# Optimization experiments

Hardware: AMD Instinct MI355X
Metric: run time of the kernel (lower is better)

The kernel has to match this reference:

```python
import jax, jax.numpy as jnp
import numpy as np

N = 100000   # nodes
E = 1600000  # edges
D_IN, D_H, D_OUT = 128, 128, 64
BN_EPS = 1e-5


def setup_inputs() -> dict:
    key = jax.random.key(0)
    ks = jax.random.split(key, 12)

    def lin_w(k, fan_in, shape):
        s = 1.0 / np.sqrt(fan_in)
        return jax.random.uniform(k, shape, jnp.float32, -s, s)

    return {
        "x": jax.random.normal(ks[0], (N, D_IN), jnp.float32),
        "edge_index": jax.random.randint(ks[1], (2, E), 0, N, dtype=jnp.int64),
        "edge_weight": jax.random.uniform(ks[2], (E,), jnp.float32),
        "W1": lin_w(ks[3], D_IN, (D_IN, D_H)),
        "b1": jnp.zeros((D_H,), jnp.float32),
        "W2": lin_w(ks[4], D_H, (D_H, D_H)),
        "b2": jnp.zeros((D_H,), jnp.float32),
        "W3": lin_w(ks[5], D_H, (D_H, D_OUT)),
        "b3": jnp.zeros((D_OUT,), jnp.float32),
        "gamma1": jnp.ones((D_H,), jnp.float32),
        "beta1": jnp.zeros((D_H,), jnp.float32),
        "gamma2": jnp.ones((D_H,), jnp.float32),
        "beta2": jnp.zeros((D_H,), jnp.float32),
    }


def _gcn_conv(x, src, dst, w, W, b):
    # PyG GCNConv: x' = D^{-1/2} (A + I) D^{-1/2} (x W) + b, self-loop weight 1
    n = x.shape[0]
    h = x @ W                                   # [N, d_out]
    loop = jnp.arange(n, dtype=src.dtype)
    s = jnp.concatenate([src, loop])            # [E+N]
    d = jnp.concatenate([dst, loop])
    ww = jnp.concatenate([w, jnp.ones((n,), w.dtype)])
    deg = jax.ops.segment_sum(ww, d, num_segments=n)          # in-degree at targets
    dinv = jnp.where(deg > 0, jax.lax.rsqrt(deg), 0.0)
    norm = dinv[s] * ww * dinv[d]               # [E+N]
    msg = h[s] * norm[:, None]                  # gather + scale
    out = jax.ops.segment_sum(msg, d, num_segments=n)
    return out + b


def _batch_norm(x, gamma, beta):
    mean = jnp.mean(x, axis=0)
    var = jnp.mean(jnp.square(x - mean), axis=0)  # biased, as BatchNorm uses
    return (x - mean) * jax.lax.rsqrt(var + BN_EPS) * gamma + beta


def reference(x, edge_index, edge_weight, W1, b1, W2, b2, W3, b3,
              gamma1, beta1, gamma2, beta2):
    src, dst = edge_index[0], edge_index[1]
    h = _gcn_conv(x, src, dst, edge_weight, W1, b1)
    h = jax.nn.relu(_batch_norm(h, gamma1, beta1))
    h = _gcn_conv(h, src, dst, edge_weight, W2, b2)
    h = jax.nn.relu(_batch_norm(h, gamma2, beta2))
    return _gcn_conv(h, src, dst, edge_weight, W3, b3)
```

## Files before the change

kernel.cpp:

```cpp
#include <hip/hip_runtime.h>
#include <hip/hip_fp16.h>
#include <cstdint>
#include <cstddef>

#define BN_EPS 1e-5f
#define FPSCALE 268435456.0f

typedef _Float16 half8 __attribute__((ext_vector_type(8)));
typedef float floatx4 __attribute__((ext_vector_type(4)));

__device__ __forceinline__ float loadS(const __half* p) { return __half2float(*p); }
__device__ __forceinline__ float2 load2(const __half* p) {
    return __half22float2(*(const __half2*)p);
}
__device__ __forceinline__ void storeS(float* p, float v) { *p = v; }
__device__ __forceinline__ void storeS(__half* p, float v) { *p = __float2half(v); }
__device__ __forceinline__ void store2(float* p, float a, float b) {
    *(float2*)p = make_float2(a, b);
}
__device__ __forceinline__ void store2(__half* p, float a, float b) {
    *(__half2*)p = __floats2half2_rn(a, b);
}
__device__ __forceinline__ float wn_of(unsigned v) {
    __half_raw hr; hr.x = (unsigned short)(v & 0x7fffu);
    return __half2float((__half)hr);
}

static __device__ __forceinline__ int load_edge(const void* ei, int mode64, long long pos) {
    if (mode64) return (int)((const long long*)ei)[pos];
    return ((const int*)ei)[pos];
}

__global__ __launch_bounds__(256) void init_kernel(const unsigned* __restrict__ eiw, int nwords,
                                                   int* __restrict__ mode,
                                                   unsigned long long* __restrict__ packed, int N,
                                                   const float* __restrict__ W1,
                                                   const float* __restrict__ W2,
                                                   const float* __restrict__ W3,
                                                   _Float16* __restrict__ WT1,
                                                   _Float16* __restrict__ WT2,
                                                   _Float16* __restrict__ WT3, int nb) {
    __shared__ unsigned red[256];
    const int bid = (int)blockIdx.x;
    const int tid = (int)threadIdx.x;
    if (bid < nb) {
        int i = bid * 256 + tid;
        if (i < N) packed[i] = 0ULL;
        return;
    }
    if (bid == nb) {
        unsigned m = 0;
        for (int i = 1 + 2 * tid; i < nwords; i += 512) m |= eiw[i];
        red[tid] = m;
        __syncthreads();
        for (int s = 128; s > 0; s >>= 1) {
            if (tid < s) red[tid] |= red[tid + s];
            __syncthreads();
        }
        if (tid == 0) mode[0] = (red[0] == 0) ? 1 : 0;
        return;
    }
    const int t_ = bid - nb - 1;
    if (t_ < 64) {
        int t = t_ * 256 + tid;
        int n = t / 128, k = t % 128;
        WT1[t] = (_Float16)W1[k * 128 + n];
    } else if (t_ < 128) {
        int t = (t_ - 64) * 256 + tid;
        int n = t / 128, k = t % 128;
        WT2[t] = (_Float16)W2[k * 128 + n];
    } else {
        int t = (t_ - 128) * 256 + tid;
        int n = t / 128, k = t % 128;
        WT3[t] = (_Float16)W3[k * 64 + n];
    }
}

template <int M, bool BN, typename TI>
__device__ __forceinline__ void gemm_body(int gbid, const TI* __restrict__ X,
                                          const _Float16* __restrict__ WTg,
                                          const float* __restrict__ sc,
                                          const float* __restrict__ sh,
                                          __half* __restrict__ Hout, int N,
                                          _Float16* WT ) {
    constexpr int CT = M / 16;
    constexpr int LDK = 136;

    for (int t = threadIdx.x; t < M * 16; t += 256) {
        int n = t / 16, seg = t % 16;
        *(half8*)&WT[n * LDK + seg * 8] = *(const half8*)&WTg[n * 128 + seg * 8];
    }
    __syncthreads();

    const int wave = (int)threadIdx.x >> 6;
    const int lane = (int)threadIdx.x & 63;
    const int qd = lane >> 4;
    const int ln = lane & 15;
    const int tile0 = gbid * 64 + wave * 16;
    int ar = tile0 + ln;
    if (ar >= N) ar = N - 1;

    half8 aF[4];
    const TI* xr = X + (size_t)ar * 128 + qd * 8;
#pragma unroll
    for (int kb = 0; kb < 4; ++kb) {
        float vv[8];
        if constexpr (sizeof(TI) == 4) {
            float4 v0 = *(const float4*)(xr + kb * 32);
            float4 v1 = *(const float4*)(xr + kb * 32 + 4);
            vv[0] = v0.x; vv[1] = v0.y; vv[2] = v0.z; vv[3] = v0.w;
            vv[4] = v1.x; vv[5] = v1.y; vv[6] = v1.z; vv[7] = v1.w;
        } else {
            half8 raw = *(const half8*)(xr + kb * 32);
#pragma unroll
            for (int j = 0; j < 8; ++j) vv[j] = (float)raw[j];
        }
        if (BN) {
            const int kbase = kb * 32 + qd * 8;
#pragma unroll
            for (int j = 0; j < 8; ++j)
                vv[j] = fmaxf(fmaf(vv[j], sc[kbase + j], sh[kbase + j]), 0.0f);
        }
        half8 a;
#pragma unroll
        for (int j = 0; j < 8; ++j) a[j] = (_Float16)vv[j];
        aF[kb] = a;
    }

#pragma unroll
    for (int ct = 0; ct < CT; ++ct) {
        floatx4 acc = {0.0f, 0.0f, 0.0f, 0.0f};
#pragma unroll
        for (int kb = 0; kb < 4; ++kb) {
            half8 b = *(const half8*)&WT[(ct * 16 + ln) * LDK + kb * 32 + qd * 8];
            acc = __builtin_amdgcn_mfma_f32_16x16x32_f16(aF[kb], b, acc, 0, 0, 0);
        }
#pragma unroll
        for (int r = 0; r < 4; ++r) {
            int orow = tile0 + qd * 4 + r;
            if (orow < N) Hout[(size_t)orow * M + ct * 16 + ln] = __float2half(acc[r]);
        }
    }
}

__global__ __launch_bounds__(256) void hist_gemm1_kernel(const void* __restrict__ ei,
                                                         const float* __restrict__ ew,
                                                         unsigned long long* __restrict__ packed,
                                                         unsigned* __restrict__ rank,
                                                         const int* __restrict__ mode, int E, int GB,
                                                         const float* __restrict__ X,
                                                         const _Float16* __restrict__ WT1g,
                                                         __half* __restrict__ Hout, int N) {
    __shared__ _Float16 WT[128 * 136];
    if ((int)blockIdx.x < GB) {
        gemm_body<128, false, float>(blockIdx.x, X, WT1g, nullptr, nullptr, Hout, N, WT);
        return;
    }
    int e = ((int)blockIdx.x - GB) * 256 + (int)threadIdx.x;
    if (e >= E) return;
    int md = *mode;
    int d = load_edge(ei, md, (long long)E + e);
    unsigned long long contrib = (1ULL << 40) | (unsigned long long)(ew[e] * FPSCALE);
    unsigned long long old = atomicAdd(&packed[d], contrib);
    rank[e] = (unsigned)(old >> 40);
}

__global__ __launch_bounds__(256) void unpack_scanA_kernel(const unsigned long long* __restrict__ packed,
                                                           float* __restrict__ dinv,
                                                           int* __restrict__ cnt,
                                                           int* __restrict__ bsum, int N) {
    __shared__ int red[256];
    const int tid = (int)threadIdx.x;
    const int base = (int)blockIdx.x * 2048 + tid * 8;
    int s = 0;
#pragma unroll
    for (int j = 0; j < 8; ++j) {
        int idx = base + j;
        if (idx < N) {
            unsigned long long p = packed[idx];
            int c = (int)(p >> 40);
            cnt[idx] = c;
            dinv[idx] = rsqrtf(1.0f + (float)(p & 0xFFFFFFFFFFULL) * (1.0f / FPSCALE));
            s += c;
        }
    }
    red[tid] = s;
    __syncthreads();
    for (int st = 128; st > 0; st >>= 1) {
        if (tid < st) red[tid] += red[tid + st];
        __syncthreads();
    }
    if (tid == 0) bsum[blockIdx.x] = red[0];
}

__global__ __launch_bounds__(256) void scanC_kernel(const int* __restrict__ cnt,
                                                    const int* __restrict__ bsum,
                                                    int* __restrict__ row_start, int N) {
    __shared__ int lds[256];
    const int tid = (int)threadIdx.x;
    int gbase = 0;
    for (int j = 0; j < (int)blockIdx.x; ++j) gbase += bsum[j];
    const int base = (int)blockIdx.x * 2048 + tid * 8;
    int vals[8];
    int s = 0;
#pragma unroll
    for (int j = 0; j < 8; ++j) {
        int idx = base + j;
        int v = (idx < N) ? cnt[idx] : 0;
        vals[j] = s;
        s += v;
    }
    lds[tid] = s;
    __syncthreads();
    for (int off = 1; off < 256; off <<= 1) {
        int t = 0;
        if (tid >= off) t = lds[tid - off];
        __syncthreads();
        lds[tid] += t;
        __syncthreads();
    }
    int excl = lds[tid] - s;
    int b = gbase + excl;
#pragma unroll
    for (int j = 0; j < 8; ++j) {
        int idx = base + j;
        if (idx < N) row_start[idx] = b + vals[j];
    }
}

__global__ __launch_bounds__(256) void scatter_zero_kernel(const void* __restrict__ ei,
                                                           const float* __restrict__ ew,
                                                           const float* __restrict__ dinv,
                                                           const int* __restrict__ row_start,
                                                           const unsigned* __restrict__ rank,
                                                           unsigned* __restrict__ edata,
                                                           const int* __restrict__ mode, int E, int EBK,
                                                           float* __restrict__ gsum,
                                                           float* __restrict__ gsq) {
    if ((int)blockIdx.x == EBK) {
        if (threadIdx.x < 128) { gsum[threadIdx.x] = 0.0f; gsq[threadIdx.x] = 0.0f; }
        return;
    }
    int e = (int)blockIdx.x * 256 + (int)threadIdx.x;
    if (e >= E) return;
    int md = *mode;
    int s = load_edge(ei, md, e);
    int d = load_edge(ei, md, (long long)E + e);
    float wn = dinv[s] * ew[e] * dinv[d];
    unsigned hb = (unsigned)__half_as_ushort(__float2half(wn)) & 0x7fffu;
    edata[row_start[d] + (int)rank[e]] = ((unsigned)s << 15) | hb;
}

template <int D, bool BIAS, typename TY>
__global__ __launch_bounds__(256) void agg_kernel(const __half* __restrict__ H,
                                                  const unsigned* __restrict__ edata,
                                                  const int* __restrict__ row_start,
                                                  const int* __restrict__ cnt,
                                                  const float* __restrict__ dinv,
                                                  const float* __restrict__ bias,
                                                  TY* __restrict__ Y, int N) {
    constexpr int VPT = D / 64;
    const int lane = (int)threadIdx.x & 63;
    const int i = (int)blockIdx.x * 4 + ((int)threadIdx.x >> 6);
    if (i >= N) return;
    const int c0 = lane * VPT;
    const float di = dinv[i];
    const float dii = di * di;

    float acc0, acc1 = 0.0f;
    if constexpr (VPT == 2) {
        float2 h = load2(H + (size_t)i * D + c0);
        acc0 = dii * h.x;
        acc1 = dii * h.y;
    } else {
        acc0 = dii * loadS(H + (size_t)i * D + c0);
    }

    const int base = row_start[i];
    const int n = cnt[i];
    for (int off = 0; off < n; off += 64) {
        const int rem = n - off;
        unsigned ev = 0;
        if (lane < rem) ev = edata[base + off + lane];
        const int mm = min(64, rem);
        for (int j = 0; j < mm; j += 8) {
            const unsigned e0 = __shfl(ev, j),     e1 = __shfl(ev, j + 1);
            const unsigned e2 = __shfl(ev, j + 2), e3 = __shfl(ev, j + 3);
            const unsigned e4 = __shfl(ev, j + 4), e5 = __shfl(ev, j + 5);
            const unsigned e6 = __shfl(ev, j + 6), e7 = __shfl(ev, j + 7);
            if constexpr (VPT == 2) {
                float2 h0 = load2(H + (size_t)(e0 >> 15) * D + c0);
                float2 h1 = load2(H + (size_t)(e1 >> 15) * D + c0);
                float2 h2 = load2(H + (size_t)(e2 >> 15) * D + c0);
                float2 h3 = load2(H + (size_t)(e3 >> 15) * D + c0);
                float2 h4 = load2(H + (size_t)(e4 >> 15) * D + c0);
                float2 h5 = load2(H + (size_t)(e5 >> 15) * D + c0);
                float2 h6 = load2(H + (size_t)(e6 >> 15) * D + c0);
                float2 h7 = load2(H + (size_t)(e7 >> 15) * D + c0);
                acc0 = fmaf(wn_of(e0), h0.x, acc0); acc1 = fmaf(wn_of(e0), h0.y, acc1);
                acc0 = fmaf(wn_of(e1), h1.x, acc0); acc1 = fmaf(wn_of(e1), h1.y, acc1);
                acc0 = fmaf(wn_of(e2), h2.x, acc0); acc1 = fmaf(wn_of(e2), h2.y, acc1);
                acc0 = fmaf(wn_of(e3), h3.x, acc0); acc1 = fmaf(wn_of(e3), h3.y, acc1);
                acc0 = fmaf(wn_of(e4), h4.x, acc0); acc1 = fmaf(wn_of(e4), h4.y, acc1);
                acc0 = fmaf(wn_of(e5), h5.x, acc0); acc1 = fmaf(wn_of(e5), h5.y, acc1);
                acc0 = fmaf(wn_of(e6), h6.x, acc0); acc1 = fmaf(wn_of(e6), h6.y, acc1);
                acc0 = fmaf(wn_of(e7), h7.x, acc0); acc1 = fmaf(wn_of(e7), h7.y, acc1);
            } else {
                float h0 = loadS(H + (size_t)(e0 >> 15) * D + c0);
                float h1 = loadS(H + (size_t)(e1 >> 15) * D + c0);
                float h2 = loadS(H + (size_t)(e2 >> 15) * D + c0);
                float h3 = loadS(H + (size_t)(e3 >> 15) * D + c0);
                float h4 = loadS(H + (size_t)(e4 >> 15) * D + c0);
                float h5 = loadS(H + (size_t)(e5 >> 15) * D + c0);
                float h6 = loadS(H + (size_t)(e6 >> 15) * D + c0);
                float h7 = loadS(H + (size_t)(e7 >> 15) * D + c0);
                acc0 = fmaf(wn_of(e0), h0, acc0);
                acc0 = fmaf(wn_of(e1), h1, acc0);
                acc0 = fmaf(wn_of(e2), h2, acc0);
                acc0 = fmaf(wn_of(e3), h3, acc0);
                acc0 = fmaf(wn_of(e4), h4, acc0);
                acc0 = fmaf(wn_of(e5), h5, acc0);
                acc0 = fmaf(wn_of(e6), h6, acc0);
                acc0 = fmaf(wn_of(e7), h7, acc0);
            }
        }
    }

    if constexpr (VPT == 2) {
        if (BIAS) { acc0 += bias[c0]; acc1 += bias[c0 + 1]; }
        store2(Y + (size_t)i * D + c0, acc0, acc1);
    } else {
        if (BIAS) acc0 += bias[c0];
        storeS(Y + (size_t)i * D + c0, acc0);
    }
}

template <int M, bool BN, typename TI, bool ZERO>
__global__ __launch_bounds__(256) void gemm_mfma_kernel(const TI* __restrict__ X,
                                                        const _Float16* __restrict__ WTg,
                                                        const float* __restrict__ sc,
                                                        const float* __restrict__ sh,
                                                        __half* __restrict__ Hout, int N,
                                                        float* __restrict__ gsum,
                                                        float* __restrict__ gsq, int GB) {
    __shared__ _Float16 WT[M * 136];
    if (ZERO && (int)blockIdx.x == GB) {
        if (threadIdx.x < 128) { gsum[threadIdx.x] = 0.0f; gsq[threadIdx.x] = 0.0f; }
        return;
    }
    gemm_body<M, BN, TI>(blockIdx.x, X, WTg, sc, sh, Hout, N, WT);
}

__global__ void stats_kernel(const __half* __restrict__ Y, float* __restrict__ gsum,
                             float* __restrict__ gsq, int N) {
    __shared__ float ls[256], lq[256];
    const int tid = threadIdx.x;
    const int c = tid & 127;
    const int half_ = tid >> 7;
    float s = 0.0f, q = 0.0f;
    for (int row = blockIdx.x * 2 + half_; row < N; row += 512) {
        float v = __half2float(Y[(size_t)row * 128 + c]);
        s += v;
        q = fmaf(v, v, q);
    }
    ls[tid] = s; lq[tid] = q;
    __syncthreads();
    if (tid < 128) {
        atomicAdd(&gsum[c], ls[tid] + ls[tid + 128]);
        atomicAdd(&gsq[c],  lq[tid] + lq[tid + 128]);
    }
}

__global__ void finalize_stats_kernel(const float* __restrict__ gsum, const float* __restrict__ gsq,
                                      const float* __restrict__ gamma, const float* __restrict__ beta,
                                      float* __restrict__ sc, float* __restrict__ sh, int N) {
    int t = threadIdx.x;
    if (t < 128) {
        float inv_n = 1.0f / (float)N;
        float mean = gsum[t] * inv_n;
        float var = gsq[t] * inv_n - mean * mean;
        float scale = gamma[t] * rsqrtf(var + BN_EPS);
        sc[t] = scale;
        sh[t] = beta[t] - mean * scale;
    }
}

extern "C" void kernel_launch(void* const* d_in, const int* in_sizes, int n_in,
                              void* d_out, int out_size, void* d_ws, size_t ws_size,
                              hipStream_t stream) {
    const float* x   = (const float*)d_in[0];
    const void*  ei  = d_in[1];
    const float* ew  = (const float*)d_in[2];
    const float* W1  = (const float*)d_in[3];
    const float* W2  = (const float*)d_in[5];
    const float* W3  = (const float*)d_in[7];
    const float* b3  = (const float*)d_in[8];
    const float* g1  = (const float*)d_in[9];
    const float* be1 = (const float*)d_in[10];
    const float* g2  = (const float*)d_in[11];
    const float* be2 = (const float*)d_in[12];
    float* out = (float*)d_out;

    const int N = in_sizes[0] / 128;
    const int E = in_sizes[2];
    const int G = (N + 2047) / 2048;

    char* w = (char*)d_ws;
    size_t off = 0;
    auto alloc = [&](size_t bytes) -> void* {
        void* p = w + off;
        off += (bytes + 255) & ~(size_t)255;
        return p;
    };
    unsigned long long* packed = (unsigned long long*)alloc((size_t)N * 8);
    float* dinv      = (float*)alloc((size_t)N * 4);
    int*   cnt       = (int*)  alloc((size_t)N * 4);
    int*   row_start = (int*)  alloc((size_t)N * 4);
    unsigned* rank   = (unsigned*)alloc((size_t)E * 4);
    unsigned* edata  = (unsigned*)alloc((size_t)E * 4);
    int*   bsum      = (int*)  alloc((size_t)G * 4);
    int*   mode      = (int*)  alloc(256);
    float* gsum      = (float*)alloc(128 * 4);
    float* gsq       = (float*)alloc(128 * 4);
    float* scb       = (float*)alloc(128 * 4);
    float* shb       = (float*)alloc(128 * 4);
    _Float16* WT1    = (_Float16*)alloc(128 * 128 * 2);
    _Float16* WT2    = (_Float16*)alloc(128 * 128 * 2);
    _Float16* WT3    = (_Float16*)alloc(128 * 64 * 2);
    __half* H        = (__half*)alloc((size_t)N * 128 * 2);
    __half* Yh       = (__half*)alloc((size_t)N * 128 * 2);
    (void)ws_size; (void)n_in; (void)out_size;

    const int nb  = (N + 255) / 256;
    const int ebk = (E + 255) / 256;
    const int gb  = (N + 63) / 64;
    const int ab  = (N + 3) / 4;

    init_kernel<<<nb + 1 + 160, 256, 0, stream>>>((const unsigned*)ei, 4096, mode, packed, N,
                                                  W1, W2, W3, WT1, WT2, WT3, nb);
    hist_gemm1_kernel<<<gb + ebk, 256, 0, stream>>>(ei, ew, packed, rank, mode, E, gb,
                                                    x, WT1, H, N);
    unpack_scanA_kernel<<<G, 256, 0, stream>>>(packed, dinv, cnt, bsum, N);
    scanC_kernel<<<G, 256, 0, stream>>>(cnt, bsum, row_start, N);
    scatter_zero_kernel<<<ebk + 1, 256, 0, stream>>>(ei, ew, dinv, row_start, rank, edata,
                                                     mode, E, ebk, gsum, gsq);

    agg_kernel<128, false, __half><<<ab, 256, 0, stream>>>(H, edata, row_start, cnt, dinv, nullptr, Yh, N);
    stats_kernel<<<256, 256, 0, stream>>>(Yh, gsum, gsq, N);
    finalize_stats_kernel<<<1, 128, 0, stream>>>(gsum, gsq, g1, be1, scb, shb, N);

    gemm_mfma_kernel<128, true, __half, true><<<gb + 1, 256, 0, stream>>>(Yh, WT2, scb, shb, H, N, gsum, gsq, gb);
    agg_kernel<128, false, __half><<<ab, 256, 0, stream>>>(H, edata, row_start, cnt, dinv, nullptr, Yh, N);
    stats_kernel<<<256, 256, 0, stream>>>(Yh, gsum, gsq, N);
    finalize_stats_kernel<<<1, 128, 0, stream>>>(gsum, gsq, g2, be2, scb, shb, N);

    gemm_mfma_kernel<64, true, __half, false><<<gb, 256, 0, stream>>>(Yh, WT3, scb, shb, H, N, nullptr, nullptr, gb);
    agg_kernel<64, true, float><<<ab, 256, 0, stream>>>(H, edata, row_start, cnt, dinv, b3, out, N);
}
```

Baseline: 550.6 us.

## Pad degree counters, vectorize histogram atomics, drop LDS from fused GEMM1

Each node's packed degree/count atomic now gets its own 64-byte slot, which is meant to cut contention and false sharing between neighbouring atomics. Each histogram thread now handles four edges with vector loads of indices, weights and rank stores. The first GEMM reads the FP16 weights straight from global memory instead of staging them in a 34KB LDS tile. That lets the kernel declare a higher occupancy hint and puts histogram blocks first in the grid. In exchange the packed array is eight times larger, so the zero-init and unpack reads become strided and touch more memory.

```diff
diff --git a/kernel.cpp b/kernel.cpp
--- a/kernel.cpp
+++ b/kernel.cpp
@@ -5,6 +5,7 @@
 
 #define BN_EPS 1e-5f
 #define FPSCALE 268435456.0f
+#define PPS 8
 
 typedef _Float16 half8 __attribute__((ext_vector_type(8)));
 typedef float floatx4 __attribute__((ext_vector_type(4)));
@@ -45,7 +46,7 @@
     const int tid = (int)threadIdx.x;
     if (bid < nb) {
         int i = bid * 256 + tid;
-        if (i < N) packed[i] = 0ULL;
+        if (i < N) packed[(size_t)i * PPS] = 0ULL;
         return;
     }
     if (bid == nb) {
@@ -143,26 +144,98 @@
     }
 }
 
-__global__ __launch_bounds__(256) void hist_gemm1_kernel(const void* __restrict__ ei,
-                                                         const float* __restrict__ ew,
-                                                         unsigned long long* __restrict__ packed,
-                                                         unsigned* __restrict__ rank,
-                                                         const int* __restrict__ mode, int E, int GB,
-                                                         const float* __restrict__ X,
-                                                         const _Float16* __restrict__ WT1g,
-                                                         __half* __restrict__ Hout, int N) {
-    __shared__ _Float16 WT[128 * 136];
-    if ((int)blockIdx.x < GB) {
-        gemm_body<128, false, float>(blockIdx.x, X, WT1g, nullptr, nullptr, Hout, N, WT);
+__device__ __forceinline__ void gemm1_nolds(int gbid, const float* __restrict__ X,
+                                            const _Float16* __restrict__ WTg,
+                                            __half* __restrict__ Hout, int N) {
+    const int wave = (int)threadIdx.x >> 6;
+    const int lane = (int)threadIdx.x & 63;
+    const int qd = lane >> 4;
+    const int ln = lane & 15;
+    const int tile0 = gbid * 64 + wave * 16;
+    int ar = tile0 + ln;
+    if (ar >= N) ar = N - 1;
+
+    half8 aF[4];
+    const float* xr = X + (size_t)ar * 128 + qd * 8;
+#pragma unroll
+    for (int kb = 0; kb < 4; ++kb) {
+        float4 v0 = *(const float4*)(xr + kb * 32);
+        float4 v1 = *(const float4*)(xr + kb * 32 + 4);
+        half8 a;
+        a[0] = (_Float16)v0.x; a[1] = (_Float16)v0.y;
+        a[2] = (_Float16)v0.z; a[3] = (_Float16)v0.w;
+        a[4] = (_Float16)v1.x; a[5] = (_Float16)v1.y;
+        a[6] = (_Float16)v1.z; a[7] = (_Float16)v1.w;
+        aF[kb] = a;
+    }
+
+#pragma unroll 1
+    for (int ct = 0; ct < 8; ++ct) {
+        floatx4 acc = {0.0f, 0.0f, 0.0f, 0.0f};
+#pragma unroll
+        for (int kb = 0; kb < 4; ++kb) {
+            half8 b = *(const half8*)&WTg[(size_t)(ct * 16 + ln) * 128 + kb * 32 + qd * 8];
+            acc = __builtin_amdgcn_mfma_f32_16x16x32_f16(aF[kb], b, acc, 0, 0, 0);
+        }
+#pragma unroll
+        for (int r = 0; r < 4; ++r) {
+            int orow = tile0 + qd * 4 + r;
+            if (orow < N) Hout[(size_t)orow * 128 + ct * 16 + ln] = __float2half(acc[r]);
+        }
+    }
+}
+
+__global__ __launch_bounds__(256, 8) void hist_gemm1_kernel(const void* __restrict__ ei,
+                                                            const float* __restrict__ ew,
+                                                            unsigned long long* __restrict__ packed,
+                                                            unsigned* __restrict__ rank,
+                                                            const int* __restrict__ mode, int E, int HB,
+                                                            const float* __restrict__ X,
+                                                            const _Float16* __restrict__ WT1g,
+                                                            __half* __restrict__ Hout, int N) {
+    if ((int)blockIdx.x >= HB) {
+        gemm1_nolds((int)blockIdx.x - HB, X, WT1g, Hout, N);
         return;
     }
-    int e = ((int)blockIdx.x - GB) * 256 + (int)threadIdx.x;
-    if (e >= E) return;
-    int md = *mode;
-    int d = load_edge(ei, md, (long long)E + e);
-    unsigned long long contrib = (1ULL << 40) | (unsigned long long)(ew[e] * FPSCALE);
-    unsigned long long old = atomicAdd(&packed[d], contrib);
-    rank[e] = (unsigned)(old >> 40);
+    const int md = *mode;
+    const int e = (int)blockIdx.x * 1024 + (int)threadIdx.x * 4;
+    if (e + 3 < E) {
+        long long d0, d1, d2, d3;
+        if (md) {
+            const long long* p = (const long long*)ei + (long long)E + e;
+            longlong2 a = *(const longlong2*)p;
+            longlong2 b = *(const longlong2*)(p + 2);
+            d0 = a.x; d1 = a.y; d2 = b.x; d3 = b.y;
+        } else {
+            const int* p = (const int*)ei + (long long)E + e;
+            int4 a = *(const int4*)p;
+            d0 = a.x; d1 = a.y; d2 = a.z; d3 = a.w;
+        }
+        float4 w4 = *(const float4*)(ew + e);
+        unsigned long long o0 = atomicAdd(&packed[(size_t)d0 * PPS],
+                                          (1ULL << 40) | (unsigned long long)(w4.x * FPSCALE));
+        unsigned long long o1 = atomicAdd(&packed[(size_t)d1 * PPS],
+                                          (1ULL << 40) | (unsigned long long)(w4.y * FPSCALE));
+        unsigned long long o2 = atomicAdd(&packed[(size_t)d2 * PPS],
+                                          (1ULL << 40) | (unsigned long long)(w4.z * FPSCALE));
+        unsigned long long o3 = atomicAdd(&packed[(size_t)d3 * PPS],
+                                          (1ULL << 40) | (unsigned long long)(w4.w * FPSCALE));
+        uint4 r4;
+        r4.x = (unsigned)(o0 >> 40); r4.y = (unsigned)(o1 >> 40);
+        r4.z = (unsigned)(o2 >> 40); r4.w = (unsigned)(o3 >> 40);
+        *(uint4*)(rank + e) = r4;
+    } else {
+#pragma unroll 1
+        for (int k = 0; k < 4; ++k) {
+            int ee = e + k;
+            if (ee >= E) break;
+            int d = load_edge(ei, md, (long long)E + ee);
+            unsigned long long contrib =
+                (1ULL << 40) | (unsigned long long)(ew[ee] * FPSCALE);
+            unsigned long long old = atomicAdd(&packed[(size_t)d * PPS], contrib);
+            rank[ee] = (unsigned)(old >> 40);
+        }
+    }
 }
 
 __global__ __launch_bounds__(256) void unpack_scanA_kernel(const unsigned long long* __restrict__ packed,
@@ -177,7 +250,7 @@
     for (int j = 0; j < 8; ++j) {
         int idx = base + j;
         if (idx < N) {
-            unsigned long long p = packed[idx];
+            unsigned long long p = packed[(size_t)idx * PPS];
             int c = (int)(p >> 40);
             cnt[idx] = c;
             dinv[idx] = rsqrtf(1.0f + (float)(p & 0xFFFFFFFFFFULL) * (1.0f / FPSCALE));
@@ -412,7 +485,7 @@
         off += (bytes + 255) & ~(size_t)255;
         return p;
     };
-    unsigned long long* packed = (unsigned long long*)alloc((size_t)N * 8);
+    unsigned long long* packed = (unsigned long long*)alloc((size_t)N * 8 * PPS);
     float* dinv      = (float*)alloc((size_t)N * 4);
     int*   cnt       = (int*)  alloc((size_t)N * 4);
     int*   row_start = (int*)  alloc((size_t)N * 4);
@@ -433,12 +506,13 @@
 
     const int nb  = (N + 255) / 256;
     const int ebk = (E + 255) / 256;
+    const int ehb = (E + 1023) / 1024;
     const int gb  = (N + 63) / 64;
     const int ab  = (N + 3) / 4;
 
     init_kernel<<<nb + 1 + 160, 256, 0, stream>>>((const unsigned*)ei, 4096, mode, packed, N,
                                                   W1, W2, W3, WT1, WT2, WT3, nb);
-    hist_gemm1_kernel<<<gb + ebk, 256, 0, stream>>>(ei, ew, packed, rank, mode, E, gb,
+    hist_gemm1_kernel<<<ehb + gb, 256, 0, stream>>>(ei, ew, packed, rank, mode, E, ehb,
                                                     x, WT1, H, N);
     unpack_scanA_kernel<<<G, 256, 0, stream>>>(packed, dinv, cnt, bsum, N);
     scanC_kernel<<<G, 256, 0, stream>>>(cnt, bsum, row_start, N);
```

Measured after the change: 581.8 us. 5.7% more time.

## Privatize degree histogram per XCC with workgroup-scope atomics

Applied to the files above, without the earlier changes.

The packed degree/count histogram is replicated into eight copies, one per XCC selected via the hardware XCC_ID register. Atomics now use workgroup scope so they can resolve in the local L2 instead of device-wide memory. Each thread also handles four edges with vector loads. The unpack step merges the copies and records per-copy prefix offsets so the scatter can compute slots, at the cost of extra zeroing, a larger workspace and an extra offset array read.

```diff
diff --git a/kernel.cpp b/kernel.cpp
--- a/kernel.cpp
+++ b/kernel.cpp
@@ -5,6 +5,7 @@
 
 #define BN_EPS 1e-5f
 #define FPSCALE 268435456.0f
+#define NCOPY 8
 
 typedef _Float16 half8 __attribute__((ext_vector_type(8)));
 typedef float floatx4 __attribute__((ext_vector_type(4)));
@@ -29,6 +30,12 @@
 static __device__ __forceinline__ int load_edge(const void* ei, int mode64, long long pos) {
     if (mode64) return (int)((const long long*)ei)[pos];
     return ((const int*)ei)[pos];
+}
+
+__device__ __forceinline__ unsigned xcc_id() {
+    unsigned v;
+    asm volatile("s_getreg_b32 %0, hwreg(HW_REG_XCC_ID)" : "=s"(v));
+    return v & 7u;
 }
 
 __global__ __launch_bounds__(256) void init_kernel(const unsigned* __restrict__ eiw, int nwords,
@@ -44,8 +51,15 @@
     const int bid = (int)blockIdx.x;
     const int tid = (int)threadIdx.x;
     if (bid < nb) {
-        int i = bid * 256 + tid;
-        if (i < N) packed[i] = 0ULL;
+        const size_t tot = (size_t)NCOPY * (size_t)N;
+        size_t i = (size_t)bid * 1024 + (size_t)tid * 4;
+        if (i + 3 < tot) {
+            *(ulonglong2*)&packed[i]     = make_ulonglong2(0ULL, 0ULL);
+            *(ulonglong2*)&packed[i + 2] = make_ulonglong2(0ULL, 0ULL);
+        } else {
+            for (int k = 0; k < 4; ++k)
+                if (i + k < tot) packed[i + k] = 0ULL;
+        }
         return;
     }
     if (bid == nb) {
@@ -156,18 +170,60 @@
         gemm_body<128, false, float>(blockIdx.x, X, WT1g, nullptr, nullptr, Hout, N, WT);
         return;
     }
-    int e = ((int)blockIdx.x - GB) * 256 + (int)threadIdx.x;
-    if (e >= E) return;
-    int md = *mode;
-    int d = load_edge(ei, md, (long long)E + e);
-    unsigned long long contrib = (1ULL << 40) | (unsigned long long)(ew[e] * FPSCALE);
-    unsigned long long old = atomicAdd(&packed[d], contrib);
-    rank[e] = (unsigned)(old >> 40);
+    const int md = *mode;
+    const unsigned xcc = xcc_id();
+    unsigned long long* __restrict__ pb = packed + (size_t)xcc * (size_t)N;
+    const int e = ((int)blockIdx.x - GB) * 1024 + (int)threadIdx.x * 4;
+    if (e + 3 < E) {
+        long long d0, d1, d2, d3;
+        if (md) {
+            const long long* p = (const long long*)ei + (long long)E + e;
+            longlong2 a = *(const longlong2*)p;
+            longlong2 b = *(const longlong2*)(p + 2);
+            d0 = a.x; d1 = a.y; d2 = b.x; d3 = b.y;
+        } else {
+            const int* p = (const int*)ei + (long long)E + e;
+            int4 a = *(const int4*)p;
+            d0 = a.x; d1 = a.y; d2 = a.z; d3 = a.w;
+        }
+        float4 w4 = *(const float4*)(ew + e);
+        unsigned long long o0 = __hip_atomic_fetch_add(
+            &pb[d0], (1ULL << 40) | (unsigned long long)(w4.x * FPSCALE),
+            __ATOMIC_RELAXED, __HIP_MEMORY_SCOPE_WORKGROUP);
+        unsigned long long o1 = __hip_atomic_fetch_add(
+            &pb[d1], (1ULL << 40) | (unsigned long long)(w4.y * FPSCALE),
+            __ATOMIC_RELAXED, __HIP_MEMORY_SCOPE_WORKGROUP);
+        unsigned long long o2 = __hip_atomic_fetch_add(
+            &pb[d2], (1ULL << 40) | (unsigned long long)(w4.z * FPSCALE),
+            __ATOMIC_RELAXED, __HIP_MEMORY_SCOPE_WORKGROUP);
+        unsigned long long o3 = __hip_atomic_fetch_add(
+            &pb[d3], (1ULL << 40) | (unsigned long long)(w4.w * FPSCALE),
+            __ATOMIC_RELAXED, __HIP_MEMORY_SCOPE_WORKGROUP);
+        uint4 r4;
+        r4.x = (xcc << 24) | (unsigned)((o0 >> 40) & 0xFFFFFFu);
+        r4.y = (xcc << 24) | (unsigned)((o1 >> 40) & 0xFFFFFFu);
+        r4.z = (xcc << 24) | (unsigned)((o2 >> 40) & 0xFFFFFFu);
+        r4.w = (xcc << 24) | (unsigned)((o3 >> 40) & 0xFFFFFFu);
+        *(uint4*)(rank + e) = r4;
+    } else {
+#pragma unroll 1
+        for (int k = 0; k < 4; ++k) {
+            int ee = e + k;
+            if (ee >= E) break;
+            int d = load_edge(ei, md, (long long)E + ee);
+            unsigned long long contrib =
+                (1ULL << 40) | (unsigned long long)(ew[ee] * FPSCALE);
+            unsigned long long old = __hip_atomic_fetch_add(
+                &pb[d], contrib, __ATOMIC_RELAXED, __HIP_MEMORY_SCOPE_WORKGROUP);
+            rank[ee] = (xcc << 24) | (unsigned)((old >> 40) & 0xFFFFFFu);
+        }
+    }
 }
 
 __global__ __launch_bounds__(256) void unpack_scanA_kernel(const unsigned long long* __restrict__ packed,
                                                            float* __restrict__ dinv,
                                                            int* __restrict__ cnt,
+                                                           unsigned* __restrict__ coff,
                                                            int* __restrict__ bsum, int N) {
     __shared__ int red[256];
     const int tid = (int)threadIdx.x;
@@ -177,11 +233,18 @@
     for (int j = 0; j < 8; ++j) {
         int idx = base + j;
         if (idx < N) {
-            unsigned long long p = packed[idx];
-            int c = (int)(p >> 40);
-            cnt[idx] = c;
-            dinv[idx] = rsqrtf(1.0f + (float)(p & 0xFFFFFFFFFFULL) * (1.0f / FPSCALE));
-            s += c;
+            unsigned long long wsum = 0ULL;
+            unsigned pref = 0;
+#pragma unroll
+            for (int c = 0; c < NCOPY; ++c) {
+                unsigned long long p = packed[(size_t)c * N + idx];
+                coff[(size_t)idx * NCOPY + c] = pref;
+                pref += (unsigned)(p >> 40);
+                wsum += (p & 0xFFFFFFFFFFULL);
+            }
+            cnt[idx] = (int)pref;
+            dinv[idx] = rsqrtf(1.0f + (float)wsum * (1.0f / FPSCALE));
+            s += (int)pref;
         }
     }
     red[tid] = s;
@@ -233,6 +296,7 @@
                                                            const float* __restrict__ dinv,
                                                            const int* __restrict__ row_start,
                                                            const unsigned* __restrict__ rank,
+                                                           const unsigned* __restrict__ coff,
                                                            unsigned* __restrict__ edata,
                                                            const int* __restrict__ mode, int E, int EBK,
                                                            float* __restrict__ gsum,
@@ -248,7 +312,11 @@
     int d = load_edge(ei, md, (long long)E + e);
     float wn = dinv[s] * ew[e] * dinv[d];
     unsigned hb = (unsigned)__half_as_ushort(__float2half(wn)) & 0x7fffu;
-    edata[row_start[d] + (int)rank[e]] = ((unsigned)s << 15) | hb;
+    unsigned r = rank[e];
+    unsigned c = r >> 24;
+    int slot = row_start[d] + (int)coff[(size_t)d * NCOPY + c] + (int)(r & 0xFFFFFFu);
+    slot = min(max(slot, 0), E - 1);
+    edata[slot] = ((unsigned)s << 15) | hb;
 }
 
 template <int D, bool BIAS, typename TY>
@@ -412,12 +480,13 @@
         off += (bytes + 255) & ~(size_t)255;
         return p;
     };
-    unsigned long long* packed = (unsigned long long*)alloc((size_t)N * 8);
+    unsigned long long* packed = (unsigned long long*)alloc((size_t)NCOPY * N * 8);
     float* dinv      = (float*)alloc((size_t)N * 4);
     int*   cnt       = (int*)  alloc((size_t)N * 4);
     int*   row_start = (int*)  alloc((size_t)N * 4);
     unsigned* rank   = (unsigned*)alloc((size_t)E * 4);
     unsigned* edata  = (unsigned*)alloc((size_t)E * 4);
+    unsigned* coff   = (unsigned*)alloc((size_t)N * NCOPY * 4);
     int*   bsum      = (int*)  alloc((size_t)G * 4);
     int*   mode      = (int*)  alloc(256);
     float* gsum      = (float*)alloc(128 * 4);
@@ -431,18 +500,19 @@
     __half* Yh       = (__half*)alloc((size_t)N * 128 * 2);
     (void)ws_size; (void)n_in; (void)out_size;
 
-    const int nb  = (N + 255) / 256;
+    const int nbz = (int)(((size_t)NCOPY * N + 1023) / 1024);
     const int ebk = (E + 255) / 256;
+    const int ehb = (E + 1023) / 1024;
     const int gb  = (N + 63) / 64;
     const int ab  = (N + 3) / 4;
 
-    init_kernel<<<nb + 1 + 160, 256, 0, stream>>>((const unsigned*)ei, 4096, mode, packed, N,
-                                                  W1, W2, W3, WT1, WT2, WT3, nb);
-    hist_gemm1_kernel<<<gb + ebk, 256, 0, stream>>>(ei, ew, packed, rank, mode, E, gb,
+    init_kernel<<<nbz + 1 + 160, 256, 0, stream>>>((const unsigned*)ei, 4096, mode, packed, N,
+                                                   W1, W2, W3, WT1, WT2, WT3, nbz);
+    hist_gemm1_kernel<<<gb + ehb, 256, 0, stream>>>(ei, ew, packed, rank, mode, E, gb,
                                                     x, WT1, H, N);
-    unpack_scanA_kernel<<<G, 256, 0, stream>>>(packed, dinv, cnt, bsum, N);
+    unpack_scanA_kernel<<<G, 256, 0, stream>>>(packed, dinv, cnt, coff, bsum, N);
     scanC_kernel<<<G, 256, 0, stream>>>(cnt, bsum, row_start, N);
-    scatter_zero_kernel<<<ebk + 1, 256, 0, stream>>>(ei, ew, dinv, row_start, rank, edata,
+    scatter_zero_kernel<<<ebk + 1, 256, 0, stream>>>(ei, ew, dinv, row_start, rank, coff, edata,
                                                      mode, E, ebk, gsum, gsq);
 
     agg_kernel<128, false, __half><<<ab, 256, 0, stream>>>(H, edata, row_start, cnt, dinv, nullptr, Yh, N);
```

After: 573.2 us. 1.04x slower.

## Build CSR via two-level bucket sort instead of global per-node atomics

Applied to the files above, without the earlier changes.

Replaces the global 64-bit atomic histogram and rank-based scatter with a coarse bucket sort. Each block first counts edges per 512-node bucket in LDS, the counts are scanned, edges are scattered into bucket order, and a per-bucket kernel builds degree, dinv, row_start and edata using LDS atomics. The edge weight stored in edata no longer includes the source dinv, so the aggregation kernels now gather dinv[src] per edge instead. This removes contended global atomics, at the cost of an extra pass over the edges, a 64-bit sorted buffer and extra dinv gathers in every aggregation.

```diff
diff --git a/kernel.cpp b/kernel.cpp
--- a/kernel.cpp
+++ b/kernel.cpp
@@ -4,7 +4,8 @@
 #include <cstddef>
 
 #define BN_EPS 1e-5f
-#define FPSCALE 268435456.0f
+#define KB 256
+#define BSH 9
 
 typedef _Float16 half8 __attribute__((ext_vector_type(8)));
 typedef float floatx4 __attribute__((ext_vector_type(4)));
@@ -33,22 +34,22 @@
 
 __global__ __launch_bounds__(256) void init_kernel(const unsigned* __restrict__ eiw, int nwords,
                                                    int* __restrict__ mode,
-                                                   unsigned long long* __restrict__ packed, int N,
+                                                   unsigned* __restrict__ pc,
                                                    const float* __restrict__ W1,
                                                    const float* __restrict__ W2,
                                                    const float* __restrict__ W3,
                                                    _Float16* __restrict__ WT1,
                                                    _Float16* __restrict__ WT2,
-                                                   _Float16* __restrict__ WT3, int nb) {
+                                                   _Float16* __restrict__ WT3) {
     __shared__ unsigned red[256];
     const int bid = (int)blockIdx.x;
     const int tid = (int)threadIdx.x;
-    if (bid < nb) {
-        int i = bid * 256 + tid;
-        if (i < N) packed[i] = 0ULL;
+    if (bid < 64) {
+        uint4 z = make_uint4(0, 0, 0, 0);
+        *(uint4*)&pc[bid * 1024 + tid * 4] = z;
         return;
     }
-    if (bid == nb) {
+    if (bid == 64) {
         unsigned m = 0;
         for (int i = 1 + 2 * tid; i < nwords; i += 512) m |= eiw[i];
         red[tid] = m;
@@ -60,7 +61,7 @@
         if (tid == 0) mode[0] = (red[0] == 0) ? 1 : 0;
         return;
     }
-    const int t_ = bid - nb - 1;
+    const int t_ = bid - 65;
     if (t_ < 64) {
         int t = t_ * 256 + tid;
         int n = t / 128, k = t % 128;
@@ -76,6 +77,65 @@
     }
 }
 
+__global__ __launch_bounds__(256) void coarse_hist_kernel(const void* __restrict__ ei,
+                                                          const int* __restrict__ mode,
+                                                          unsigned* __restrict__ pc,
+                                                          int E, int epb) {
+    __shared__ unsigned h[256];
+    const int k = (int)blockIdx.x;
+    const int tid = (int)threadIdx.x;
+    h[tid] = 0;
+    __syncthreads();
+    const int md = *mode;
+    const int e0 = k * epb;
+    const int e1 = min(E, e0 + epb);
+    for (int e = e0 + tid; e < e1; e += 256) {
+        int d = load_edge(ei, md, (long long)E + e);
+        atomicAdd(&h[d >> BSH], 1u);
+    }
+    __syncthreads();
+    pc[k * 256 + tid] = h[tid];
+}
+
+__global__ __launch_bounds__(256) void scan_pc_kernel(unsigned* __restrict__ pc,
+                                                      int* __restrict__ tb) {
+    __shared__ int red[256];
+    const int b = (int)blockIdx.x;
+    const int tid = (int)threadIdx.x;
+    const unsigned v = pc[tid * 256 + b];
+    red[tid] = (int)v;
+    __syncthreads();
+    for (int off = 1; off < 256; off <<= 1) {
+        int t = 0;
+        if (tid >= off) t = red[tid - off];
+        __syncthreads();
+        red[tid] += t;
+        __syncthreads();
+    }
+    pc[tid * 256 + b] = (unsigned)(red[tid] - (int)v);
+    if (tid == 255) tb[b] = red[255];
+}
+
+__global__ __launch_bounds__(256) void scan_buckets_kernel(const int* __restrict__ tb,
+                                                           int* __restrict__ bbase, int nbuck,
+                                                           float* __restrict__ gsum,
+                                                           float* __restrict__ gsq) {
+    __shared__ int red[256];
+    const int tid = (int)threadIdx.x;
+    const int v = (tid < nbuck) ? tb[tid] : 0;
+    red[tid] = v;
+    __syncthreads();
+    for (int off = 1; off < 256; off <<= 1) {
+        int t = 0;
+        if (tid >= off) t = red[tid - off];
+        __syncthreads();
+        red[tid] += t;
+        __syncthreads();
+    }
+    bbase[tid] = red[tid] - v;
+    if (tid < 128) { gsum[tid] = 0.0f; gsq[tid] = 0.0f; }
+}
+
 template <int M, bool BN, typename TI>
 __device__ __forceinline__ void gemm_body(int gbid, const TI* __restrict__ X,
                                           const _Float16* __restrict__ WTg,
@@ -143,112 +203,113 @@
     }
 }
 
-__global__ __launch_bounds__(256) void hist_gemm1_kernel(const void* __restrict__ ei,
+__global__ __launch_bounds__(256) void sort_gemm1_kernel(const void* __restrict__ ei,
                                                          const float* __restrict__ ew,
-                                                         unsigned long long* __restrict__ packed,
-                                                         unsigned* __restrict__ rank,
-                                                         const int* __restrict__ mode, int E, int GB,
+                                                         const unsigned* __restrict__ pc,
+                                                         const int* __restrict__ bbase,
+                                                         unsigned long long* __restrict__ sortedE,
+                                                         const int* __restrict__ mode, int E,
+                                                         int epb, int GB,
                                                          const float* __restrict__ X,
                                                          const _Float16* __restrict__ WT1g,
                                                          __half* __restrict__ Hout, int N) {
     __shared__ _Float16 WT[128 * 136];
+    __shared__ unsigned off_s[256];
     if ((int)blockIdx.x < GB) {
         gemm_body<128, false, float>(blockIdx.x, X, WT1g, nullptr, nullptr, Hout, N, WT);
         return;
     }
-    int e = ((int)blockIdx.x - GB) * 256 + (int)threadIdx.x;
-    if (e >= E) return;
-    int md = *mode;
-    int d = load_edge(ei, md, (long long)E + e);
-    unsigned long long contrib = (1ULL << 40) | (unsigned long long)(ew[e] * FPSCALE);
-    unsigned long long old = atomicAdd(&packed[d], contrib);
-    rank[e] = (unsigned)(old >> 40);
-}
-
-__global__ __launch_bounds__(256) void unpack_scanA_kernel(const unsigned long long* __restrict__ packed,
-                                                           float* __restrict__ dinv,
-                                                           int* __restrict__ cnt,
-                                                           int* __restrict__ bsum, int N) {
+    const int k = (int)blockIdx.x - GB;
+    const int tid = (int)threadIdx.x;
+    off_s[tid] = (unsigned)bbase[tid] + pc[k * 256 + tid];
+    __syncthreads();
+    const int md = *mode;
+    const int e0 = k * epb;
+    const int e1 = min(E, e0 + epb);
+    for (int e = e0 + tid; e < e1; e += 256) {
+        int d = load_edge(ei, md, (long long)E + e);
+        int s = load_edge(ei, md, e);
+        float wv = ew[e];
+        unsigned slot = atomicAdd(&off_s[d >> BSH], 1u);
+        sortedE[slot] = ((unsigned long long)(unsigned)d << 33) |
+                        ((unsigned long long)(unsigned)s << 16) |
+                        (unsigned long long)(unsigned short)__half_as_ushort(__float2half(wv));
+    }
+}
+
+__global__ __launch_bounds__(256) void csr_build_kernel(const unsigned long long* __restrict__ sortedE,
+                                                        const int* __restrict__ bbase,
+                                                        const int* __restrict__ tb,
+                                                        float* __restrict__ dinv,
+                                                        int* __restrict__ cnt,
+                                                        int* __restrict__ row_start,
+                                                        unsigned* __restrict__ edata, int N) {
+    __shared__ unsigned cs[512];
+    __shared__ float ws[512];
+    __shared__ float dv[512];
+    __shared__ unsigned sc[512];
+    __shared__ unsigned cur[512];
     __shared__ int red[256];
+    const int b = (int)blockIdx.x;
     const int tid = (int)threadIdx.x;
-    const int base = (int)blockIdx.x * 2048 + tid * 8;
-    int s = 0;
-#pragma unroll
-    for (int j = 0; j < 8; ++j) {
-        int idx = base + j;
-        if (idx < N) {
-            unsigned long long p = packed[idx];
-            int c = (int)(p >> 40);
-            cnt[idx] = c;
-            dinv[idx] = rsqrtf(1.0f + (float)(p & 0xFFFFFFFFFFULL) * (1.0f / FPSCALE));
-            s += c;
-        }
-    }
-    red[tid] = s;
-    __syncthreads();
-    for (int st = 128; st > 0; st >>= 1) {
-        if (tid < st) red[tid] += red[tid + st];
-        __syncthreads();
-    }
-    if (tid == 0) bsum[blockIdx.x] = red[0];
-}
-
-__global__ __launch_bounds__(256) void scanC_kernel(const int* __restrict__ cnt,
-                                                    const int* __restrict__ bsum,
-                                                    int* __restrict__ row_start, int N) {
-    __shared__ int lds[256];
-    const int tid = (int)threadIdx.x;
-    int gbase = 0;
-    for (int j = 0; j < (int)blockIdx.x; ++j) gbase += bsum[j];
-    const int base = (int)blockIdx.x * 2048 + tid * 8;
-    int vals[8];
-    int s = 0;
-#pragma unroll
-    for (int j = 0; j < 8; ++j) {
-        int idx = base + j;
-        int v = (idx < N) ? cnt[idx] : 0;
-        vals[j] = s;
-        s += v;
-    }
-    lds[tid] = s;
+    const int n0 = b << BSH;
+    const int base = bbase[b];
+    const int len = tb[b];
+
+    cs[tid] = 0; cs[tid + 256] = 0;
+    ws[tid] = 0.0f; ws[tid + 256] = 0.0f;
+    cur[tid] = 0; cur[tid + 256] = 0;
+    __syncthreads();
+
+    for (int i = tid; i < len; i += 256) {
+        unsigned long long p = sortedE[base + i];
+        unsigned fine = (unsigned)(p >> 33) - (unsigned)n0;
+        atomicAdd(&cs[fine], 1u);
+        __half_raw hr; hr.x = (unsigned short)(p & 0xFFFFu);
+        atomicAdd(&ws[fine], __half2float((__half)hr));
+    }
+    __syncthreads();
+
+    const unsigned a0 = cs[2 * tid];
+    const unsigned a1 = cs[2 * tid + 1];
+    const int s2 = (int)(a0 + a1);
+    red[tid] = s2;
     __syncthreads();
     for (int off = 1; off < 256; off <<= 1) {
         int t = 0;
-        if (tid >= off) t = lds[tid - off];
-        __syncthreads();
-        lds[tid] += t;
-        __syncthreads();
-    }
-    int excl = lds[tid] - s;
-    int b = gbase + excl;
-#pragma unroll
-    for (int j = 0; j < 8; ++j) {
-        int idx = base + j;
-        if (idx < N) row_start[idx] = b + vals[j];
-    }
-}
-
-__global__ __launch_bounds__(256) void scatter_zero_kernel(const void* __restrict__ ei,
-                                                           const float* __restrict__ ew,
-                                                           const float* __restrict__ dinv,
-                                                           const int* __restrict__ row_start,
-                                                           const unsigned* __restrict__ rank,
-                                                           unsigned* __restrict__ edata,
-                                                           const int* __restrict__ mode, int E, int EBK,
-                                                           float* __restrict__ gsum,
-                                                           float* __restrict__ gsq) {
-    if ((int)blockIdx.x == EBK) {
-        if (threadIdx.x < 128) { gsum[threadIdx.x] = 0.0f; gsq[threadIdx.x] = 0.0f; }
-        return;
-    }
-    int e = (int)blockIdx.x * 256 + (int)threadIdx.x;
-    if (e >= E) return;
-    int md = *mode;
-    int s = load_edge(ei, md, e);
-    int d = load_edge(ei, md, (long long)E + e);
-    float wn = dinv[s] * ew[e] * dinv[d];
-    unsigned hb = (unsigned)__half_as_ushort(__float2half(wn)) & 0x7fffu;
-    edata[row_start[d] + (int)rank[e]] = ((unsigned)s << 15) | hb;
+        if (tid >= off) t = red[tid - off];
+        __syncthreads();
+        red[tid] += t;
+        __syncthreads();
+    }
+    const int excl2 = red[tid] - s2;
+    sc[2 * tid] = (unsigned)excl2;
+    sc[2 * tid + 1] = (unsigned)(excl2 + (int)a0);
+
+#pragma unroll
+    for (int q = 0; q < 2; ++q) {
+        const int f = tid + q * 256;
+        const int node = n0 + f;
+        const float dvv = rsqrtf(1.0f + ws[f]);
+        dv[f] = dvv;
+        if (node < N) {
+            dinv[node] = dvv;
+            cnt[node] = (int)cs[f];
+            row_start[node] = base + (int)sc[f];
+        }
+    }
+    __syncthreads();
+
+    for (int i = tid; i < len; i += 256) {
+        unsigned long long p = sortedE[base + i];
+        unsigned fine = (unsigned)(p >> 33) - (unsigned)n0;
+        unsigned s = (unsigned)(p >> 16) & 0x1FFFFu;
+        __half_raw hr; hr.x = (unsigned short)(p & 0xFFFFu);
+        float wnp = __half2float((__half)hr) * dv[fine];
+        unsigned r = atomicAdd(&cur[fine], 1u);
+        unsigned hb = (unsigned)__half_as_ushort(__float2half(wnp)) & 0x7fffu;
+        edata[base + (int)sc[fine] + (int)r] = (s << 15) | hb;
+    }
 }
 
 template <int D, bool BIAS, typename TY>
@@ -288,6 +349,14 @@
             const unsigned e2 = __shfl(ev, j + 2), e3 = __shfl(ev, j + 3);
             const unsigned e4 = __shfl(ev, j + 4), e5 = __shfl(ev, j + 5);
             const unsigned e6 = __shfl(ev, j + 6), e7 = __shfl(ev, j + 7);
+            const float w0 = dinv[e0 >> 15] * wn_of(e0);
+            const float w1 = dinv[e1 >> 15] * wn_of(e1);
+            const float w2 = dinv[e2 >> 15] * wn_of(e2);
+            const float w3 = dinv[e3 >> 15] * wn_of(e3);
+            const float w4 = dinv[e4 >> 15] * wn_of(e4);
+            const float w5 = dinv[e5 >> 15] * wn_of(e5);
+            const float w6 = dinv[e6 >> 15] * wn_of(e6);
+            const float w7 = dinv[e7 >> 15] * wn_of(e7);
             if constexpr (VPT == 2) {
                 float2 h0 = load2(H + (size_t)(e0 >> 15) * D + c0);
                 float2 h1 = load2(H + (size_t)(e1 >> 15) * D + c0);
@@ -297,14 +366,14 @@
                 float2 h5 = load2(H + (size_t)(e5 >> 15) * D + c0);
                 float2 h6 = load2(H + (size_t)(e6 >> 15) * D + c0);
                 float2 h7 = load2(H + (size_t)(e7 >> 15) * D + c0);
-                acc0 = fmaf(wn_of(e0), h0.x, acc0); acc1 = fmaf(wn_of(e0), h0.y, acc1);
-                acc0 = fmaf(wn_of(e1), h1.x, acc0); acc1 = fmaf(wn_of(e1), h1.y, acc1);
-                acc0 = fmaf(wn_of(e2), h2.x, acc0); acc1 = fmaf(wn_of(e2), h2.y, acc1);
-                acc0 = fmaf(wn_of(e3), h3.x, acc0); acc1 = fmaf(wn_of(e3), h3.y, acc1);
-                acc0 = fmaf(wn_of(e4), h4.x, acc0); acc1 = fmaf(wn_of(e4), h4.y, acc1);
-                acc0 = fmaf(wn_of(e5), h5.x, acc0); acc1 = fmaf(wn_of(e5), h5.y, acc1);
-                acc0 = fmaf(wn_of(e6), h6.x, acc0); acc1 = fmaf(wn_of(e6), h6.y, acc1);
-                acc0 = fmaf(wn_of(e7), h7.x, acc0); acc1 = fmaf(wn_of(e7), h7.y, acc1);
+                acc0 = fmaf(w0, h0.x, acc0); acc1 = fmaf(w0, h0.y, acc1);
+                acc0 = fmaf(w1, h1.x, acc0); acc1 = fmaf(w1, h1.y, acc1);
+                acc0 = fmaf(w2, h2.x, acc0); acc1 = fmaf(w2, h2.y, acc1);
+                acc0 = fmaf(w3, h3.x, acc0); acc1 = fmaf(w3, h3.y, acc1);
+                acc0 = fmaf(w4, h4.x, acc0); acc1 = fmaf(w4, h4.y, acc1);
+                acc0 = fmaf(w5, h5.x, acc0); acc1 = fmaf(w5, h5.y, acc1);
+                acc0 = fmaf(w6, h6.x, acc0); acc1 = fmaf(w6, h6.y, acc1);
+                acc0 = fmaf(w7, h7.x, acc0); acc1 = fmaf(w7, h7.y, acc1);
             } else {
                 float h0 = loadS(H + (size_t)(e0 >> 15) * D + c0);
                 float h1 = loadS(H + (size_t)(e1 >> 15) * D + c0);
@@ -314,14 +383,14 @@
                 float h5 = loadS(H + (size_t)(e5 >> 15) * D + c0);
                 float h6 = loadS(H + (size_t)(e6 >> 15) * D + c0);
                 float h7 = loadS(H + (size_t)(e7 >> 15) * D + c0);
-                acc0 = fmaf(wn_of(e0), h0, acc0);
-                acc0 = fmaf(wn_of(e1), h1, acc0);
-                acc0 = fmaf(wn_of(e2), h2, acc0);
-                acc0 = fmaf(wn_of(e3), h3, acc0);
-                acc0 = fmaf(wn_of(e4), h4, acc0);
-                acc0 = fmaf(wn_of(e5), h5, acc0);
-                acc0 = fmaf(wn_of(e6), h6, acc0);
-                acc0 = fmaf(wn_of(e7), h7, acc0);
+                acc0 = fmaf(w0, h0, acc0);
+                acc0 = fmaf(w1, h1, acc0);
+                acc0 = fmaf(w2, h2, acc0);
+                acc0 = fmaf(w3, h3, acc0);
+                acc0 = fmaf(w4, h4, acc0);
+                acc0 = fmaf(w5, h5, acc0);
+                acc0 = fmaf(w6, h6, acc0);
+                acc0 = fmaf(w7, h7, acc0);
             }
         }
     }
@@ -403,7 +472,6 @@
 
     const int N = in_sizes[0] / 128;
     const int E = in_sizes[2];
-    const int G = (N + 2047) / 2048;
 
     char* w = (char*)d_ws;
     size_t off = 0;
@@ -412,13 +480,14 @@
         off += (bytes + 255) & ~(size_t)255;
         return p;
     };
-    unsigned long long* packed = (unsigned long long*)alloc((size_t)N * 8);
+    unsigned* pc     = (unsigned*)alloc(256 * 256 * 4);
+    int*   tb        = (int*)  alloc(256 * 4);
+    int*   bbase     = (int*)  alloc(256 * 4);
+    unsigned long long* sortedE = (unsigned long long*)alloc((size_t)E * 8);
     float* dinv      = (float*)alloc((size_t)N * 4);
     int*   cnt       = (int*)  alloc((size_t)N * 4);
     int*   row_start = (int*)  alloc((size_t)N * 4);
-    unsigned* rank   = (unsigned*)alloc((size_t)E * 4);
     unsigned* edata  = (unsigned*)alloc((size_t)E * 4);
-    int*   bsum      = (int*)  alloc((size_t)G * 4);
     int*   mode      = (int*)  alloc(256);
     float* gsum      = (float*)alloc(128 * 4);
     float* gsq       = (float*)alloc(128 * 4);
@@ -431,19 +500,20 @@
     __half* Yh       = (__half*)alloc((size_t)N * 128 * 2);
     (void)ws_size; (void)n_in; (void)out_size;
 
-    const int nb  = (N + 255) / 256;
-    const int ebk = (E + 255) / 256;
-    const int gb  = (N + 63) / 64;
-    const int ab  = (N + 3) / 4;
-
-    init_kernel<<<nb + 1 + 160, 256, 0, stream>>>((const unsigned*)ei, 4096, mode, packed, N,
-                                                  W1, W2, W3, WT1, WT2, WT3, nb);
-    hist_gemm1_kernel<<<gb + ebk, 256, 0, stream>>>(ei, ew, packed, rank, mode, E, gb,
-                                                    x, WT1, H, N);
-    unpack_scanA_kernel<<<G, 256, 0, stream>>>(packed, dinv, cnt, bsum, N);
-    scanC_kernel<<<G, 256, 0, stream>>>(cnt, bsum, row_start, N);
-    scatter_zero_kernel<<<ebk + 1, 256, 0, stream>>>(ei, ew, dinv, row_start, rank, edata,
-                                                     mode, E, ebk, gsum, gsq);
+    const int epb   = (E + KB - 1) / KB;
+    const int nbuck = (N + (1 << BSH) - 1) >> BSH;
+    const int gb    = (N + 63) / 64;
+    const int ab    = (N + 3) / 4;
+
+    init_kernel<<<64 + 1 + 160, 256, 0, stream>>>((const unsigned*)ei, 4096, mode, pc,
+                                                  W1, W2, W3, WT1, WT2, WT3);
+    coarse_hist_kernel<<<KB, 256, 0, stream>>>(ei, mode, pc, E, epb);
+    scan_pc_kernel<<<nbuck, 256, 0, stream>>>(pc, tb);
+    scan_buckets_kernel<<<1, 256, 0, stream>>>(tb, bbase, nbuck, gsum, gsq);
+    sort_gemm1_kernel<<<gb + KB, 256, 0, stream>>>(ei, ew, pc, bbase, sortedE, mode, E,
+                                                   epb, gb, x, WT1, H, N);
+    csr_build_kernel<<<nbuck, 256, 0, stream>>>(sortedE, bbase, tb, dinv, cnt, row_start,
+                                                edata, N);
 
     agg_kernel<128, false, __half><<<ab, 256, 0, stream>>>(H, edata, row_start, cnt, dinv, nullptr, Yh, N);
     stats_kernel<<<256, 256, 0, stream>>>(Yh, gsum, gsq, N);
```

After: 498.9 us. -9.4%, faster.
